# Kernel tuning notes

Measured on AMD Instinct MI355X. Metric: run time of the kernel, lower is better.

The kernel has to match this reference:

```python
import jax, jax.numpy as jnp
import numpy as np
from jax import lax

V_JOINTS = 25
N_SCALES = 13
C1 = 96
N_SEG = 50
EPS = 1e-5

# NTU RGB+D 25-joint skeleton edges (0-indexed)
_EDGES = [(0,1),(1,20),(2,20),(3,2),(4,20),(5,4),(6,5),(7,6),(8,20),(9,8),
          (10,9),(11,10),(12,0),(13,12),(14,13),(15,14),(16,0),(17,16),
          (18,17),(19,18),(21,22),(22,7),(23,24),(24,11)]


def _build_A_powers():
    # MS-G3D disentangled multi-scale adjacency: k-hop shells, D^-1/2 A D^-1/2 normalized
    A = np.zeros((V_JOINTS, V_JOINTS), dtype=np.float64)
    for i, j in _EDGES:
        A[i, j] = 1.0
        A[j, i] = 1.0
    I = np.eye(V_JOINTS)
    mats = []
    for k in range(N_SCALES):
        if k == 0:
            Ak = I.copy()
        else:
            Ak = (np.minimum(np.linalg.matrix_power(A + I, k), 1)
                  - np.minimum(np.linalg.matrix_power(A + I, k - 1), 1))
            Ak = Ak + I  # with_self=True
        d = Ak.sum(-1)
        Dinv = np.diag(d ** -0.5)
        mats.append(Dinv @ Ak @ Dinv)
    return np.concatenate(mats, axis=0).astype(np.float32)  # (13*25, 25)


def _segments(T, n_seg):
    # Segment boundaries exactly as the torch code: int(round(linspace(1, T, n_seg+1)))
    t_vec = [int(round(v)) for v in np.linspace(1, T, n_seg + 1)]
    lens = [t_vec[i + 1] - t_vec[i] for i in range(n_seg)]
    L = max(lens)
    idx = np.zeros((n_seg, L), dtype=np.int32)
    mask = np.zeros((n_seg, L), dtype=np.float32)
    for s in range(n_seg):
        start = t_vec[s] - 1
        for l in range(L):
            idx[s, l] = min(start + l, T - 2)
            mask[s, l] = 1.0 if l < lens[s] else 0.0
    sp_idx = np.array([t - 1 for t in t_vec[:-1]], dtype=np.int32)
    return idx, mask, sp_idx


def setup_inputs() -> dict:
    key = jax.random.key(0)
    ks = jax.random.split(key, 18)
    N, M, C, T, V = 4, 2, 3, 300, V_JOINTS
    num_classes = 60
    Cbn = M * C * V                       # 150
    Dlog = C1 + C1 * (C1 - 1) // 2        # 4656 (depth-2 logsig dims)
    Din = C1 + Dlog                       # 4752 (start pos + logsig)
    f = lambda k, s: jax.random.normal(k, s, dtype=jnp.float32)
    return {
        'x': f(ks[0], (N, M, C, T, V)),
        'bn_g': 1.0 + 0.1 * f(ks[1], (Cbn,)),
        'bn_b': 0.1 * f(ks[2], (Cbn,)),
        'bn_m': 0.1 * f(ks[3], (Cbn,)),
        'bn_v': jax.random.uniform(ks[4], (Cbn,), minval=0.5, maxval=1.5),
        'A_powers': jnp.asarray(_build_A_powers()),
        'A_res': jax.random.uniform(ks[5], (N_SCALES * V, V), minval=-1e-6, maxval=1e-6),
        'W_gcn': f(ks[6], (C1, N_SCALES * C)) / np.sqrt(N_SCALES * C),
        'b_gcn': 0.1 * f(ks[7], (C1,)),
        'bn2_g': 1.0 + 0.1 * f(ks[8], (C1,)),
        'bn2_b': 0.1 * f(ks[9], (C1,)),
        'bn2_m': 0.1 * f(ks[10], (C1,)),
        'bn2_v': jax.random.uniform(ks[11], (C1,), minval=0.5, maxval=1.5),
        'W_ih': f(ks[12], (4 * C1, Din)) / np.sqrt(Din),
        'W_hh': f(ks[13], (4 * C1, C1)) / np.sqrt(C1),
        'b_ih': 0.1 * f(ks[14], (4 * C1,)),
        'b_hh': 0.1 * f(ks[15], (4 * C1,)),
        'W_fc': f(ks[16], (num_classes, C1)) / np.sqrt(C1),
        'b_fc': 0.1 * f(ks[17], (num_classes,)),
    }


def reference(x, bn_g, bn_b, bn_m, bn_v, A_powers, A_res, W_gcn, b_gcn,
              bn2_g, bn2_b, bn2_m, bn2_v, W_ih, W_hh, b_ih, b_hh, W_fc, b_fc):
    N, M, C, T, V = x.shape
    NM = N * M
    # --- data_bn (inference BatchNorm1d over M*V*C channels) ---
    xb = x.transpose(0, 1, 4, 2, 3).reshape(N, M * V * C, T)
    xb = (xb - bn_m[:, None]) * (bn_g / jnp.sqrt(bn_v + EPS))[:, None] + bn_b[:, None]
    xg = xb.reshape(NM, V, C, T).transpose(0, 2, 3, 1)          # (NM, C, T, V)
    # --- MS_GCN: multi-scale disentangled graph conv ---
    A = A_powers + A_res                                        # (S*V, V)
    sup = jnp.einsum('vu,nctu->nctv', A, xg)                    # (NM, C, T, S*V)
    sup = sup.reshape(NM, C, T, N_SCALES, V).transpose(0, 3, 1, 2, 4)
    sup = sup.reshape(NM, N_SCALES * C, T, V)
    y = jnp.einsum('oc,nctv->notv', W_gcn, sup) + b_gcn[None, :, None, None]
    y = (y - bn2_m[None, :, None, None]) * (bn2_g / jnp.sqrt(bn2_v + EPS))[None, :, None, None] \
        + bn2_b[None, :, None, None]
    y = jax.nn.relu(y)                                          # (NM, C1, T, V)
    # --- LogSigRNN: per-joint temporal path, depth-2 log-signature per segment ---
    p = y.transpose(0, 3, 2, 1).reshape(NM * V, T, C1)          # (B, T, C1)
    idx, mask, sp_idx = _segments(T, N_SEG)
    dx = jnp.diff(p, axis=1)                                    # (B, T-1, C1)
    dseg = dx[:, idx] * mask[None, :, :, None]                  # (B, nseg, L, C1)
    pseg = jnp.cumsum(dseg, axis=2) - dseg                      # exclusive prefix within segment
    s1 = dseg.sum(axis=2)                                       # level-1: total increment
    Q = jnp.einsum('bslc,bsld->bscd', pseg, dseg)               # (B, nseg, C1, C1)
    levy = 0.5 * (Q - jnp.swapaxes(Q, -1, -2))                  # level-2 (Levy area)
    iu, ju = np.triu_indices(C1, 1)
    ls2 = levy[:, :, iu, ju]                                    # (B, nseg, 4560)
    start_pos = p[:, sp_idx, :]                                 # (B, nseg, C1)
    feat = jnp.concatenate([start_pos, s1, ls2], axis=-1)       # (B, nseg, 4752)
    # --- LSTM (torch gate order i,f,g,o) ---
    B = feat.shape[0]
    xw = jnp.einsum('btd,gd->btg', feat, W_ih) + (b_ih + b_hh)
    def step(carry, xt):
        h, c = carry
        g = xt + h @ W_hh.T
        i, fg, gg, o = jnp.split(g, 4, axis=-1)
        c = jax.nn.sigmoid(fg) * c + jax.nn.sigmoid(i) * jnp.tanh(gg)
        h = jax.nn.sigmoid(o) * jnp.tanh(c)
        return (h, c), h
    h0 = jnp.zeros((B, C1), feat.dtype)
    _, hs = lax.scan(step, (h0, h0), jnp.swapaxes(xw, 0, 1))
    hs = jnp.swapaxes(hs, 0, 1)                                 # (B, nseg, C1)
    out = hs.reshape(NM, V, N_SEG, C1).transpose(0, 3, 2, 1)    # (NM, C1, nseg, V)
    out = out.reshape(N, M, C1, -1).mean(axis=3).mean(axis=1)   # (N, C1)
    return out @ W_fc.T + b_fc
```

## Files before the change

### kernel.cpp

```cpp
#include <hip/hip_runtime.h>
#include <math.h>

#define KF 4752
#define KP 4768
#define KSTEPS 149
#define G4 384
#define NPAIR 4560
#define EPSBN 1e-5f
#define XWHALF 3840000

typedef float f32x4 __attribute__((ext_vector_type(4)));
typedef short s16x8 __attribute__((ext_vector_type(8)));

__device__ __forceinline__ unsigned short f2bf(float x){
  unsigned u = __float_as_uint(x);
  return (unsigned short)((u + 0x7fffu + ((u>>16)&1u)) >> 16);
}
__device__ __forceinline__ float bf2f(unsigned short h){
  return __uint_as_float(((unsigned)h)<<16);
}

__device__ __forceinline__ int seg_start(int s){ return (s<=24)? 6*s : 149 + 6*(s-25); }
__device__ __forceinline__ int seg_len(int s){ return (s==24)?5:6; }

__global__ void kGeff(const float* bn_g, const float* bn_v,
                      const float* Ap, const float* Ar, const float* Wg,
                      const float* bn2_g, const float* bn2_v, float* geffT){
  int idx = blockIdx.x*256 + threadIdx.x;
  if (idx >= 2*96*25*75) return;
  int cu = idx % 75; int rest = idx/75;
  int v = rest % 25; rest /= 25;
  int o = rest % 96; int m = rest / 96;
  int c = cu/25, u = cu%25;
  int ch = (m*25+u)*3 + c;
  float s1 = bn_g[ch] / sqrtf(bn_v[ch] + EPSBN);
  float s2 = bn2_g[o] / sqrtf(bn2_v[o] + EPSBN);
  float acc = 0.f;
  for (int k=0;k<13;k++){
    float a = Ap[(k*25+v)*25+u] + Ar[(k*25+v)*25+u];
    acc += Wg[o*39 + k*3 + c] * a;
  }
  geffT[((size_t)(m*75+cu))*2400 + v*96 + o] = acc * s1 * s2;
}

__global__ __launch_bounds__(256) void kBeff(const float* bn_g,const float* bn_b,const float* bn_m,const float* bn_v,
                      const float* Ap,const float* Ar,const float* Wg,const float* bg,
                      const float* bn2_g,const float* bn2_b,const float* bn2_m,const float* bn2_v,
                      float* beffT){
  int wid  = (blockIdx.x*256 + threadIdx.x) >> 6;
  int lane = threadIdx.x & 63;
  if (wid >= 2*96*25) return;
  int v = wid % 25; int rest = wid/25; int o = rest % 96; int m = rest/96;
  float acc = 0.f;
  #pragma unroll
  for (int it=0; it<16; ++it){
    int item = it*64 + lane;
    if (item < 975){
      int k = item / 75; int cu = item % 75; int c = cu/25, u = cu%25;
      int ch = (m*25+u)*3 + c;
      float s1 = bn_g[ch] / sqrtf(bn_v[ch] + EPSBN);
      float t1 = bn_b[ch] - bn_m[ch]*s1;
      float a  = Ap[(k*25+v)*25+u] + Ar[(k*25+v)*25+u];
      acc += Wg[o*39 + k*3 + c] * a * t1;
    }
  }
  #pragma unroll
  for (int off=32; off; off>>=1) acc += __shfl_down(acc, off);
  if (lane == 0){
    acc += bg[o];
    float s2 = bn2_g[o]/sqrtf(bn2_v[o]+EPSBN);
    beffT[m*2400 + v*96 + o] = s2*(acc - bn2_m[o]) + bn2_b[o];
  }
}

__global__ void kPairs(int* pairs){
  int k = blockIdx.x*256+threadIdx.x;
  if (k >= NPAIR) return;
  int i=0, rem=k;
  while (rem >= 95 - i){ rem -= (95 - i); i++; }
  int j = i + 1 + rem;
  pairs[k] = (i<<7) | j;
}

__global__ void kWsplit(const float* w, unsigned short* whi, unsigned short* wlo){
  int idx = blockIdx.x*256 + threadIdx.x;
  if (idx >= G4*KP) return;
  int g = idx / KP, k = idx % KP;
  float v = (k < KF) ? w[(size_t)g*KF + k] : 0.f;
  unsigned short h = f2bf(v);
  whi[idx] = h;
  wlo[idx] = f2bf(v - bf2f(h));
}

#define TTILE 10
__global__ __launch_bounds__(256) void kP(const float* x, const float* geffT, const float* beffT, float* p){
  int nm = blockIdx.y;
  int t0 = blockIdx.x * TTILE;
  int m  = nm % 2;
  __shared__ float xs[75*TTILE];
  int tid = threadIdx.x;
  for (int li = tid; li < 75*TTILE; li += 256){
    int u = li % 25; int rest = li/25; int tt = rest % TTILE; int c = rest / TTILE;
    xs[(c*25+u)*TTILE + tt] = x[(((size_t)nm*3 + c)*300 + (t0+tt))*25 + u];
  }
  __syncthreads();
  const float* gT = geffT + (size_t)m*75*2400;
  for (int ow = tid; ow < 2400; ow += 256){
    int o = ow % 96, v = ow / 96;
    float b = beffT[m*2400 + ow];
    float acc[TTILE];
    #pragma unroll
    for (int t=0;t<TTILE;t++) acc[t] = b;
    for (int cu=0; cu<75; cu++){
      float gv = gT[(size_t)cu*2400 + ow];
      #pragma unroll
      for (int t=0;t<TTILE;t++) acc[t] += gv * xs[cu*TTILE+t];
    }
    #pragma unroll
    for (int t=0;t<TTILE;t++)
      p[((size_t)(nm*25+v)*300 + t0+t)*96 + o] = fmaxf(acc[t], 0.f);
  }
}

__global__ __launch_bounds__(256) void kFeat(const float* p, const int* pairs,
                                             unsigned short* fhi, unsigned short* flo, int row0){
  int row = row0 + blockIdx.x;
  int b = row / 50, s = row % 50;
  int S = seg_start(s), len = seg_len(s);
  __shared__ float ps[6][96];
  __shared__ float ds[6][96];
  int tid = threadIdx.x;
  size_t base = (size_t)blockIdx.x * KP;
  if (tid < 96){
    int c = tid;
    float pv[7];
    #pragma unroll
    for (int l=0;l<7;l++) pv[l] = p[((size_t)b*300 + S + l)*96 + c];
    float run = 0.f;
    #pragma unroll
    for (int l=0;l<6;l++){
      float d = (l < len) ? (pv[l+1]-pv[l]) : 0.f;
      ps[l][c] = run; ds[l][c] = d; run += d;
    }
    unsigned short h0 = f2bf(pv[0]);
    fhi[base + c] = h0; flo[base + c] = f2bf(pv[0] - bf2f(h0));
    unsigned short h1 = f2bf(run);
    fhi[base + 96 + c] = h1; flo[base + 96 + c] = f2bf(run - bf2f(h1));
  } else if (tid < 112){
    int c = KF + (tid - 96);
    fhi[base + c] = 0; flo[base + c] = 0;
  }
  __syncthreads();
  for (int k = tid; k < NPAIR; k += 256){
    int pr = pairs[k];
    int i = pr >> 7, j = pr & 127;
    float q = 0.f;
    #pragma unroll
    for (int l=0;l<6;l++) q += ps[l][i]*ds[l][j] - ps[l][j]*ds[l][i];
    q *= 0.5f;
    unsigned short h = f2bf(q);
    fhi[base + 192 + k] = h; flo[base + 192 + k] = f2bf(q - bf2f(h));
  }
}

__device__ __forceinline__ void gload16(const void* g, void* l){
  __builtin_amdgcn_global_load_lds(
      (const __attribute__((address_space(1))) void*)g,
      (__attribute__((address_space(3))) void*)l, 16, 0, 0);
}

__global__ __launch_bounds__(256) void kGemm(
    const unsigned short* __restrict__ fhi, const unsigned short* __restrict__ flo,
    const unsigned short* __restrict__ whi, const unsigned short* __restrict__ wlo,
    float* __restrict__ xw, int chunkRow0, int nrows)
{
  __shared__ unsigned short lds[2][20480];
  int tid  = threadIdx.x;
  int lane = tid & 63, w = tid >> 6;
  int colBase = blockIdx.x * 192;
  int zz      = blockIdx.y;
  int mblk    = blockIdx.z;
  int zbase   = zz * 75;
  int zSteps  = zz ? (KSTEPS - 75) : 75;

  const unsigned short* gptr[10];
  int ldsOff[10];
  #pragma unroll
  for (int q=0;q<10;q++){
    int c = (w*10 + q)*64 + lane;
    const unsigned short* bp; int rr;
    if (c < 512)        { rr = c;        bp = fhi + (size_t)(mblk*128 + (rr>>2))*KP; }
    else if (c < 1024)  { rr = c-512;    bp = flo + (size_t)(mblk*128 + (rr>>2))*KP; }
    else if (c < 1792)  { rr = c-1024;   bp = whi + (size_t)(colBase  + (rr>>2))*KP; }
    else                { rr = c-1792;   bp = wlo + (size_t)(colBase  + (rr>>2))*KP; }
    int row = rr>>2, gl = rr&3;
    int gs = gl ^ ((row>>1)&3);
    gptr[q]  = bp + gs*8;
    ldsOff[q] = (w*10 + q)*512;
  }

  int wm = w & 1, wn = w >> 1;
  int gsel = lane >> 4;
  int aoff[4], boff[6];
  #pragma unroll
  for (int fm=0; fm<4; fm++){
    int r = wm*64 + fm*16 + (lane&15);
    aoff[fm] = r*32 + ((gsel ^ ((r>>1)&3))*8);
  }
  #pragma unroll
  for (int fn=0; fn<6; fn++){
    int r = wn*96 + fn*16 + (lane&15);
    boff[fn] = 8192 + r*32 + ((gsel ^ ((r>>1)&3))*8);
  }

  f32x4 acc[4][6];
  #pragma unroll
  for (int fm=0;fm<4;fm++)
    #pragma unroll
    for (int fn=0;fn<6;fn++) acc[fm][fn] = (f32x4){0.f,0.f,0.f,0.f};

  #pragma unroll
  for (int q=0;q<10;q++) gload16(gptr[q] + (size_t)zbase*32, &lds[0][ldsOff[q]]);

  int cur = 0;
  for (int t=0; t<zSteps; ++t){
    __syncthreads();
    if (t+1 < zSteps){
      size_t ko = (size_t)(zbase + t + 1)*32;
      #pragma unroll
      for (int q=0;q<10;q++) gload16(gptr[q] + ko, &lds[cur^1][ldsOff[q]]);
    }
    const unsigned short* L = lds[cur];
    s16x8 ah[4], al[4], bh[6], bl[6];
    #pragma unroll
    for (int fm=0;fm<4;fm++){
      ah[fm] = *(const s16x8*)(L + aoff[fm]);
      al[fm] = *(const s16x8*)(L + aoff[fm] + 4096);
    }
    #pragma unroll
    for (int fn=0;fn<6;fn++){
      bh[fn] = *(const s16x8*)(L + boff[fn]);
      bl[fn] = *(const s16x8*)(L + boff[fn] + 6144);
    }
    #pragma unroll
    for (int fm=0;fm<4;fm++)
      #pragma unroll
      for (int fn=0;fn<6;fn++){
        acc[fm][fn] = __builtin_amdgcn_mfma_f32_16x16x32_bf16(ah[fm], bh[fn], acc[fm][fn], 0,0,0);
        acc[fm][fn] = __builtin_amdgcn_mfma_f32_16x16x32_bf16(ah[fm], bl[fn], acc[fm][fn], 0,0,0);
        acc[fm][fn] = __builtin_amdgcn_mfma_f32_16x16x32_bf16(al[fm], bh[fn], acc[fm][fn], 0,0,0);
      }
    cur ^= 1;
  }

  int rl = (lane>>4)*4, cl = lane&15;
  float* outp = xw + (size_t)zz*XWHALF;
  #pragma unroll
  for (int fm=0;fm<4;fm++){
    #pragma unroll
    for (int fn=0;fn<6;fn++){
      int gr0 = mblk*128 + wm*64 + fm*16 + rl;
      int gc  = colBase + wn*96 + fn*16 + cl;
      f32x4 v = acc[fm][fn];
      #pragma unroll
      for (int r=0;r<4;r++){
        int gr = gr0 + r;
        if (gr < nrows)
          outp[(size_t)(chunkRow0 + gr)*G4 + gc] = v[r];
      }
    }
  }
}

__global__ __launch_bounds__(384) void kLstm(const float* xw, const float* whh,
                                             const float* bih, const float* bhh, float* hsum){
  int b = blockIdx.x;
  int g = threadIdx.x;
  __shared__ __align__(16) float h_s[96];
  __shared__ float gbuf[384];
  float wreg[96];
  #pragma unroll
  for (int k=0;k<96;k++) wreg[k] = whh[(size_t)g*96 + k];
  float breg = bih[g] + bhh[g];
  float cval = 0.f, hacc = 0.f;
  if (g < 96) h_s[g] = 0.f;
  __syncthreads();
  const float* xrow  = xw + (size_t)b*50*G4;
  const float* xrow2 = xrow + XWHALF;
  for (int t=0;t<50;t++){
    float acc = xrow[t*G4 + g] + xrow2[t*G4 + g] + breg;
    #pragma unroll
    for (int k=0;k<96;k+=4){
      float4 h4 = *(const float4*)&h_s[k];
      acc += wreg[k]*h4.x + wreg[k+1]*h4.y + wreg[k+2]*h4.z + wreg[k+3]*h4.w;
    }
    gbuf[g] = acc;
    __syncthreads();
    if (g < 96){
      float ig = gbuf[g], fg = gbuf[96+g], gg = gbuf[192+g], og = gbuf[288+g];
      float si = 1.f/(1.f+expf(-ig));
      float sf = 1.f/(1.f+expf(-fg));
      float so = 1.f/(1.f+expf(-og));
      cval = sf*cval + si*tanhf(gg);
      float h = so * tanhf(cval);
      h_s[g] = h;
      hacc += h;
    }
    __syncthreads();
  }
  if (g < 96) hsum[(size_t)b*96 + g] = hacc;
}

__global__ void kOut(const float* hsum, const float* wfc, const float* bfc, float* out){
  int n = blockIdx.x;
  __shared__ float pool[96];
  int tid = threadIdx.x;
  if (tid < 96){
    float a = 0.f;
    for (int mv=0; mv<50; mv++) a += hsum[((size_t)(n*50 + mv))*96 + tid];
    pool[tid] = a / 2500.f;
  }
  __syncthreads();
  if (tid < 60){
    float a = bfc[tid];
    for (int o=0;o<96;o++) a += pool[o]*wfc[tid*96+o];
    out[n*60+tid] = a;
  }
}

extern "C" void kernel_launch(void* const* d_in, const int* in_sizes, int n_in,
                              void* d_out, int out_size, void* d_ws, size_t ws_size,
                              hipStream_t stream){
  const float* x     = (const float*)d_in[0];
  const float* bn_g  = (const float*)d_in[1];
  const float* bn_b  = (const float*)d_in[2];
  const float* bn_m  = (const float*)d_in[3];
  const float* bn_v  = (const float*)d_in[4];
  const float* Ap    = (const float*)d_in[5];
  const float* Ar    = (const float*)d_in[6];
  const float* Wg    = (const float*)d_in[7];
  const float* bg    = (const float*)d_in[8];
  const float* bn2_g = (const float*)d_in[9];
  const float* bn2_b = (const float*)d_in[10];
  const float* bn2_m = (const float*)d_in[11];
  const float* bn2_v = (const float*)d_in[12];
  const float* wih   = (const float*)d_in[13];
  const float* whh   = (const float*)d_in[14];
  const float* bih   = (const float*)d_in[15];
  const float* bhh   = (const float*)d_in[16];
  const float* wfc   = (const float*)d_in[17];
  const float* bfc   = (const float*)d_in[18];
  float* out = (float*)d_out;

  float* ws    = (float*)d_ws;
  float* geffT = ws;
  float* beffT = geffT + 360000;
  int*   pairs = (int*)(beffT + 4800);
  float* pbuf  = beffT + 4800 + 4560;
  float* xw    = pbuf + 5760000;
  float* hsum  = xw + 2*XWHALF;
  unsigned short* whiP = (unsigned short*)(hsum + 19200);
  unsigned short* wloP = whiP + (size_t)G4*KP;
  unsigned short* fhi  = wloP + (size_t)G4*KP;
  size_t fixedFloats = 360000u + 4800u + 4560u + 5760000u + 2u*XWHALF + 19200u
                     + (size_t)G4*KP;
  long long availB = (long long)ws_size - (long long)(fixedFloats*4);
  long long perBlk128 = 128LL*KP*2*2;
  int blocks128 = (availB > 0) ? (int)(availB / perBlk128) : 1;
  if (blocks128 < 1)  blocks128 = 1;
  if (blocks128 > 79) blocks128 = 79;
  int chunkRows = blocks128 * 128;
  unsigned short* flo = fhi + (size_t)chunkRows*KP;

  kGeff<<<(2*96*25*75 + 255)/256, 256, 0, stream>>>(bn_g, bn_v, Ap, Ar, Wg, bn2_g, bn2_v, geffT);
  kBeff<<<1200, 256, 0, stream>>>(bn_g, bn_b, bn_m, bn_v, Ap, Ar, Wg, bg,
                                  bn2_g, bn2_b, bn2_m, bn2_v, beffT);
  kPairs<<<(NPAIR + 255)/256, 256, 0, stream>>>(pairs);
  kWsplit<<<((G4*KP) + 255)/256, 256, 0, stream>>>(wih, whiP, wloP);
  kP<<<dim3(30, 8), 256, 0, stream>>>(x, geffT, beffT, pbuf);

  for (int r0 = 0; r0 < 10000; r0 += chunkRows){
    int nr = 10000 - r0; if (nr > chunkRows) nr = chunkRows;
    kFeat<<<nr, 256, 0, stream>>>(pbuf, pairs, fhi, flo, r0);
    kGemm<<<dim3(2, 2, (nr + 127)/128), 256, 0, stream>>>(fhi, flo, whiP, wloP, xw, r0, nr);
  }

  kLstm<<<200, 384, 0, stream>>>(xw, whh, bih, bhh, hsum);
  kOut<<<4, 128, 0, stream>>>(hsum, wfc, bfc, out);
}
```

Baseline: 397.7 us.

## Split GEMM K into four slices, widen kFeat blocks, split kP output range

The GEMM's split-K factor rises from 2 to 4, so four partial xw buffers are written and the LSTM sums all four. This raises the block count on the many-CU GPU. kFeat moves to 512 threads, and each thread now computes two Levy-area pairs with packed 32-bit stores. kP gains a z dimension that splits its output columns across two blocks. The costs are more workspace for xw partials, which can shrink the feature chunk size, and more partial-sum traffic.

After: 458.0 us. 15.2% more time.

```diff
diff --git a/kernel.cpp b/kernel.cpp
--- a/kernel.cpp
+++ b/kernel.cpp
@@ -97,6 +97,7 @@
   int nm = blockIdx.y;
   int t0 = blockIdx.x * TTILE;
   int m  = nm % 2;
+  int half = blockIdx.z;
   __shared__ float xs[75*TTILE];
   int tid = threadIdx.x;
   for (int li = tid; li < 75*TTILE; li += 256){
@@ -105,7 +106,7 @@
   }
   __syncthreads();
   const float* gT = geffT + (size_t)m*75*2400;
-  for (int ow = tid; ow < 2400; ow += 256){
+  for (int ow = half*1200 + tid; ow < (half+1)*1200; ow += 256){
     int o = ow % 96, v = ow / 96;
     float b = beffT[m*2400 + ow];
     float acc[TTILE];
@@ -122,7 +123,7 @@
   }
 }
 
-__global__ __launch_bounds__(256) void kFeat(const float* p, const int* pairs,
+__global__ __launch_bounds__(512) void kFeat(const float* p, const int* pairs,
                                              unsigned short* fhi, unsigned short* flo, int row0){
   int row = row0 + blockIdx.x;
   int b = row / 50, s = row % 50;
@@ -151,15 +152,23 @@
     fhi[base + c] = 0; flo[base + c] = 0;
   }
   __syncthreads();
-  for (int k = tid; k < NPAIR; k += 256){
-    int pr = pairs[k];
-    int i = pr >> 7, j = pr & 127;
-    float q = 0.f;
-    #pragma unroll
-    for (int l=0;l<6;l++) q += ps[l][i]*ds[l][j] - ps[l][j]*ds[l][i];
-    q *= 0.5f;
-    unsigned short h = f2bf(q);
-    fhi[base + 192 + k] = h; flo[base + 192 + k] = f2bf(q - bf2f(h));
+  unsigned* hi32 = (unsigned*)(fhi + base + 192);
+  unsigned* lo32 = (unsigned*)(flo + base + 192);
+  for (int pk = tid; pk < NPAIR/2; pk += 512){
+    int pr0 = pairs[2*pk], pr1 = pairs[2*pk+1];
+    int i0 = pr0 >> 7, j0 = pr0 & 127;
+    int i1 = pr1 >> 7, j1 = pr1 & 127;
+    float q0 = 0.f, q1 = 0.f;
+    #pragma unroll
+    for (int l=0;l<6;l++){
+      q0 += ps[l][i0]*ds[l][j0] - ps[l][j0]*ds[l][i0];
+      q1 += ps[l][i1]*ds[l][j1] - ps[l][j1]*ds[l][i1];
+    }
+    q0 *= 0.5f; q1 *= 0.5f;
+    unsigned short h0 = f2bf(q0), h1 = f2bf(q1);
+    hi32[pk] = (unsigned)h0 | ((unsigned)h1 << 16);
+    unsigned short l0 = f2bf(q0 - bf2f(h0)), l1 = f2bf(q1 - bf2f(h1));
+    lo32[pk] = (unsigned)l0 | ((unsigned)l1 << 16);
   }
 }
 
@@ -180,8 +189,8 @@
   int colBase = blockIdx.x * 192;
   int zz      = blockIdx.y;
   int mblk    = blockIdx.z;
-  int zbase   = zz * 75;
-  int zSteps  = zz ? (KSTEPS - 75) : 75;
+  int zbase   = (zz==0) ? 0 : (38 + 37*(zz-1));
+  int zSteps  = (zz==0) ? 38 : 37;
 
   const unsigned short* gptr[10];
   int ldsOff[10];
@@ -285,10 +294,11 @@
   float cval = 0.f, hacc = 0.f;
   if (g < 96) h_s[g] = 0.f;
   __syncthreads();
-  const float* xrow  = xw + (size_t)b*50*G4;
-  const float* xrow2 = xrow + XWHALF;
+  const float* xr0 = xw + (size_t)b*50*G4;
   for (int t=0;t<50;t++){
-    float acc = xrow[t*G4 + g] + xrow2[t*G4 + g] + breg;
+    int o = t*G4 + g;
+    float acc = xr0[o] + xr0[XWHALF + o] + xr0[2*(size_t)XWHALF + o]
+              + xr0[3*(size_t)XWHALF + o] + breg;
     #pragma unroll
     for (int k=0;k<96;k+=4){
       float4 h4 = *(const float4*)&h_s[k];
@@ -358,11 +368,11 @@
   int*   pairs = (int*)(beffT + 4800);
   float* pbuf  = beffT + 4800 + 4560;
   float* xw    = pbuf + 5760000;
-  float* hsum  = xw + 2*XWHALF;
+  float* hsum  = xw + 4*(size_t)XWHALF;
   unsigned short* whiP = (unsigned short*)(hsum + 19200);
   unsigned short* wloP = whiP + (size_t)G4*KP;
   unsigned short* fhi  = wloP + (size_t)G4*KP;
-  size_t fixedFloats = 360000u + 4800u + 4560u + 5760000u + 2u*XWHALF + 19200u
+  size_t fixedFloats = 360000u + 4800u + 4560u + 5760000u + 4u*(size_t)XWHALF + 19200u
                      + (size_t)G4*KP;
   long long availB = (long long)ws_size - (long long)(fixedFloats*4);
   long long perBlk128 = 128LL*KP*2*2;
@@ -377,12 +387,12 @@
                                   bn2_g, bn2_b, bn2_m, bn2_v, beffT);
   kPairs<<<(NPAIR + 255)/256, 256, 0, stream>>>(pairs);
   kWsplit<<<((G4*KP) + 255)/256, 256, 0, stream>>>(wih, whiP, wloP);
-  kP<<<dim3(30, 8), 256, 0, stream>>>(x, geffT, beffT, pbuf);
+  kP<<<dim3(30, 8, 2), 256, 0, stream>>>(x, geffT, beffT, pbuf);
 
   for (int r0 = 0; r0 < 10000; r0 += chunkRows){
     int nr = 10000 - r0; if (nr > chunkRows) nr = chunkRows;
-    kFeat<<<nr, 256, 0, stream>>>(pbuf, pairs, fhi, flo, r0);
-    kGemm<<<dim3(2, 2, (nr + 127)/128), 256, 0, stream>>>(fhi, flo, whiP, wloP, xw, r0, nr);
+    kFeat<<<nr, 512, 0, stream>>>(pbuf, pairs, fhi, flo, r0);
+    kGemm<<<dim3(2, 4, (nr + 127)/128), 256, 0, stream>>>(fhi, flo, whiP, wloP, xw, r0, nr);
   }
 
   kLstm<<<200, 384, 0, stream>>>(xw, whh, bih, bhh, hsum);
```
